# Kernel optimization log

Hardware: AMD Instinct MI355X
Metric: run time of the kernel (lower is better)

Reference implementation:

```python
import jax, jax.numpy as jnp
import numpy as np

CTX = 5  # context_len

def z_vector(x, ctx):
    # x: [B, L, E] -> [B, L, ctx*E]; slot j holds embedding of token (idx + j - ctx//2), zero-padded at edges
    half = ctx // 2
    B, L, E = x.shape
    xp = jnp.pad(x, ((0, 0), (half, half), (0, 0)))
    return jnp.concatenate([xp[:, i:i + L, :] for i in range(ctx)], axis=-1)

def setup_inputs() -> dict:
    key = jax.random.key(0)
    kq, ka, kw, kb = jax.random.split(key, 4)
    B, LQ, LA, E, F = 256, 64, 256, 300, 512
    question = jax.random.normal(kq, (B, LQ, E), dtype=jnp.float32)
    answer = jax.random.normal(ka, (B, LA, E), dtype=jnp.float32)
    W = jax.random.normal(kw, (CTX * E, F), dtype=jnp.float32) * 0.02
    b = jax.random.normal(kb, (F,), dtype=jnp.float32) * 0.02
    return {"question": question, "answer": answer, "W": W, "b": b}

def reference(question, answer, W, b):
    # Conv2d(1, F, (ctx*E, 1)) over the full-height Z vector == per-position linear map
    def branch(x):
        z = z_vector(x, CTX)                       # [B, L, ctx*E]
        out = jnp.einsum('blk,kf->bfl', z, W)      # [B, F, L]
        return out + b[None, :, None]
    return branch(question), branch(answer)
```

## Files before the change

kernel.cpp:

```cpp
#include <hip/hip_runtime.h>

#define NB   256
#define E0   300
#define EP   304
#define F_   512
#define KP   1536
#define NKT  48
#define LQ_  64
#define LA_  256

typedef __attribute__((ext_vector_type(4))) float f32x4;
typedef __attribute__((ext_vector_type(8))) short short8;

#define XQ_ELEMS (NB * (LQ_ + 4) * EP)
#define XA_ELEMS (NB * (LA_ + 4) * EP)
#define WF_ELEMS (F_ * KP)
#define OUTQ_ELEMS ((size_t)NB * F_ * LQ_)

__device__ __forceinline__ unsigned short f2bf(float x) {
    unsigned int u = __float_as_uint(x);
    u = u + 0x7fffu + ((u >> 16) & 1u);
    return (unsigned short)(u >> 16);
}

__global__ void prep_x(const float* __restrict__ q, const float* __restrict__ a,
                       unsigned short* __restrict__ xq, unsigned short* __restrict__ xa)
{
    const int row = blockIdx.x;
    const int tid = threadIdx.x;
    if (tid >= 76) return;
    const float* src;
    unsigned short* dst;
    bool valid;
    if (row < NB * (LQ_ + 4)) {
        int b = row / (LQ_ + 4), lp = row - b * (LQ_ + 4);
        dst = xq + (size_t)row * EP;
        valid = (lp >= 2 && lp < 2 + LQ_);
        src = q + ((size_t)b * LQ_ + (lp - 2)) * E0;
    } else {
        int r2 = row - NB * (LQ_ + 4);
        int b = r2 / (LA_ + 4), lp = r2 - b * (LA_ + 4);
        dst = xa + (size_t)r2 * EP;
        valid = (lp >= 2 && lp < 2 + LA_);
        src = a + ((size_t)b * LA_ + (lp - 2)) * E0;
    }
    unsigned long long pk = 0ull;
    if (valid && tid < 75) {
        const float4 v = reinterpret_cast<const float4*>(src)[tid];
        pk = (unsigned long long)f2bf(v.x)
           | ((unsigned long long)f2bf(v.y) << 16)
           | ((unsigned long long)f2bf(v.z) << 32)
           | ((unsigned long long)f2bf(v.w) << 48);
    }
    *reinterpret_cast<unsigned long long*>(dst + (size_t)tid * 4) = pk;
}

__global__ void prep_w2(const float* __restrict__ W, unsigned short* __restrict__ wfr)
{
    int idx = blockIdx.x * 256 + threadIdx.x;
    int j    = idx & 7;
    int lane = (idx >> 3) & 63;
    int chunk = idx >> 9;
    int kc = chunk % NKT;
    int tile16 = chunk / NKT;
    int f  = tile16 * 16 + (lane & 15);
    int kp = kc * 32 + (lane >> 4) * 8 + j;
    int jj = kp / EP;
    int e  = kp - jj * EP;
    float v = (kp < 5 * EP && e < E0) ? W[(size_t)(jj * E0 + e) * F_ + f] : 0.f;
    wfr[idx] = f2bf(v);
}

__global__ __launch_bounds__(256, 2) void qa_gemm(
    const unsigned short* __restrict__ xq,
    const unsigned short* __restrict__ xa,
    const unsigned short* __restrict__ wfr,
    const float* __restrict__ bias,
    float* __restrict__ out)
{
    __shared__ __align__(16) unsigned short lds[4 * 4096];

    const int bid = blockIdx.x;
    const int wg  = (bid & 7) * 160 + (bid >> 3);

    const unsigned short* xp;
    float* ob;
    int Mbase, lsh, Lp, ftBase;
    if (wg < 256) {
        Mbase  = (wg >> 1) * 128;
        ftBase = (wg & 1) * 256;
        xp = xq; lsh = 6; Lp = LQ_ + 4;
        ob = out;
    } else {
        const int id = wg - 256;
        Mbase  = (id >> 1) * 128;
        ftBase = (id & 1) * 256;
        xp = xa; lsh = 8; Lp = LA_ + 4;
        ob = out + OUTQ_ELEMS;
    }
    const int Lv = 1 << lsh;

    const int tid  = threadIdx.x;
    const int lane = tid & 63;
    const int wid  = tid >> 6;
    const int lq   = lane >> 4;
    const int lr   = lane & 15;

    const int s_c  = (lane & 3) ^ ((lane >> 3) & 3);
    const int sub  = lane >> 2;
    const int mr0 = Mbase + wid * 32 + sub, mr1 = mr0 + 16;
    const unsigned short* gZ0 = xp + (size_t)((mr0 >> lsh) * Lp + (mr0 & (Lv - 1))) * EP + s_c * 8;
    const unsigned short* gZ1 = xp + (size_t)((mr1 >> lsh) * Lp + (mr1 & (Lv - 1))) * EP + s_c * 8;
    const int dz0 = wid * 1024, dz1 = dz0 + 512;

#define GLLDS(p, d) __builtin_amdgcn_global_load_lds(                               \
        (const __attribute__((address_space(1))) void*)(p),                         \
        (__attribute__((address_space(3))) void*)(d), 16, 0, 0)
#define STAGE_Z(T) do { const int rb = ((T) & 3) * 4096; const size_t ko = (size_t)(T) * 32; \
    GLLDS(gZ0 + ko, lds + dz0 + rb); GLLDS(gZ1 + ko, lds + dz1 + rb); } while (0)

    const unsigned short* wpc0 = wfr + (size_t)((ftBase >> 4) + wid * 4 + 0) * NKT * 512 + lane * 8;
    const unsigned short* wpc1 = wfr + (size_t)((ftBase >> 4) + wid * 4 + 1) * NKT * 512 + lane * 8;
    const unsigned short* wpc2 = wfr + (size_t)((ftBase >> 4) + wid * 4 + 2) * NKT * 512 + lane * 8;
    const unsigned short* wpc3 = wfr + (size_t)((ftBase >> 4) + wid * 4 + 3) * NKT * 512 + lane * 8;

#define WLOAD(dst, p) do {                                                           \
    asm volatile("global_load_dwordx4 %0, %1, off" : "=v"(dst) : "v"(p) : "memory"); \
    (p) += 512; } while (0)

    const int cs = (lq ^ ((lr >> 1) & 3)) * 16;
    int zoff[8];
#pragma unroll
    for (int n = 0; n < 8; ++n) zoff[n] = (n * 16 + lr) * 64 + cs;

    f32x4 acc[4][8] = {};
    short8 WA0, WA1, WA2, WA3, WB0, WB1, WB2, WB3;

#define MFMA(a, b, c) __builtin_amdgcn_mfma_f32_16x16x32_bf16((a), (b), (c), 0, 0, 0)

#define KSTEP(T, C0, C1, C2, C3, N0, N1, N2, N3, DO_W, DO_Z, MIDW) do {             \
    const char* bb = (const char*)lds + ((T) & 3) * 8192;                           \
    short8 bA[4], bB[4];                                                            \
    _Pragma("unroll") for (int n = 0; n < 4; ++n) bA[n] = *(const short8*)(bb + zoff[n]); \
    if (DO_W) { WLOAD(N0, wpc0); WLOAD(N1, wpc1); WLOAD(N2, wpc2); WLOAD(N3, wpc3); } \
    if (DO_Z) { STAGE_Z((T) + 3); }                                                 \
    asm volatile("s_barrier\n\ts_waitcnt vmcnt(" #MIDW ") lgkmcnt(0)" ::: "memory"); \
    __builtin_amdgcn_sched_barrier(0);                                              \
    __builtin_amdgcn_s_setprio(1);                                                  \
    _Pragma("unroll") for (int n = 0; n < 4; ++n) {                                 \
        acc[0][n] = MFMA(C0, bA[n], acc[0][n]);                                     \
        acc[1][n] = MFMA(C1, bA[n], acc[1][n]);                                     \
        acc[2][n] = MFMA(C2, bA[n], acc[2][n]);                                     \
        acc[3][n] = MFMA(C3, bA[n], acc[3][n]);                                     \
    }                                                                               \
    __builtin_amdgcn_s_setprio(0);                                                  \
    __builtin_amdgcn_sched_barrier(0);                                              \
    _Pragma("unroll") for (int n = 0; n < 4; ++n) bB[n] = *(const short8*)(bb + zoff[4 + n]); \
    asm volatile("s_barrier\n\ts_waitcnt lgkmcnt(0)" ::: "memory");                 \
    __builtin_amdgcn_sched_barrier(0);                                              \
    __builtin_amdgcn_s_setprio(1);                                                  \
    _Pragma("unroll") for (int n = 0; n < 4; ++n) {                                 \
        acc[0][4 + n] = MFMA(C0, bB[n], acc[0][4 + n]);                             \
        acc[1][4 + n] = MFMA(C1, bB[n], acc[1][4 + n]);                             \
        acc[2][4 + n] = MFMA(C2, bB[n], acc[2][4 + n]);                             \
        acc[3][4 + n] = MFMA(C3, bB[n], acc[3][4 + n]);                             \
    }                                                                               \
    __builtin_amdgcn_s_setprio(0);                                                  \
    __builtin_amdgcn_sched_barrier(0);                                              \
} while (0)

#define ENDFENCE(N) asm volatile("s_waitcnt vmcnt(" #N ")\n\ts_barrier" ::: "memory")

    WLOAD(WA0, wpc0); WLOAD(WA1, wpc1); WLOAD(WA2, wpc2); WLOAD(WA3, wpc3);
    STAGE_Z(0); STAGE_Z(1); STAGE_Z(2);
    ENDFENCE(4);

    for (int i = 0; i < 22; ++i) {
        const int t = 2 * i;
        KSTEP(t,     WA0, WA1, WA2, WA3, WB0, WB1, WB2, WB3, 1, 1, 8);
        ENDFENCE(12);
        KSTEP(t + 1, WB0, WB1, WB2, WB3, WA0, WA1, WA2, WA3, 1, 1, 8);
        ENDFENCE(12);
    }
    KSTEP(44, WA0, WA1, WA2, WA3, WB0, WB1, WB2, WB3, 1, 1, 8);
    ENDFENCE(12);
    KSTEP(45, WB0, WB1, WB2, WB3, WA0, WA1, WA2, WA3, 1, 0, 6);
    ENDFENCE(10);
    KSTEP(46, WA0, WA1, WA2, WA3, WB0, WB1, WB2, WB3, 1, 0, 4);
    ENDFENCE(8);
    KSTEP(47, WB0, WB1, WB2, WB3, WA0, WA1, WA2, WA3, 0, 0, 0);

#undef KSTEP
#undef ENDFENCE
#undef WLOAD
#undef STAGE_Z
#undef GLLDS
#undef MFMA

#pragma unroll
    for (int ns = 0; ns < 8; ++ns) {
        const int m = Mbase + ns * 16 + lr;
        const int b = m >> lsh;
        const int l = m & (Lv - 1);
        float* orow = ob + ((size_t)b * F_ << lsh) + l;
#pragma unroll
        for (int ms = 0; ms < 4; ++ms) {
            const int f0 = ftBase + wid * 64 + ms * 16 + lq * 4;
            const f32x4 v = acc[ms][ns];
#pragma unroll
            for (int r = 0; r < 4; ++r)
                orow[(size_t)(f0 + r) << lsh] = v[r] + __ldg(&bias[f0 + r]);
        }
    }
}

extern "C" void kernel_launch(void* const* d_in, const int* in_sizes, int n_in,
                              void* d_out, int out_size, void* d_ws, size_t ws_size,
                              hipStream_t stream)
{
    const float* q    = (const float*)d_in[0];
    const float* a    = (const float*)d_in[1];
    const float* W    = (const float*)d_in[2];
    const float* bias = (const float*)d_in[3];
    float* out = (float*)d_out;

    unsigned short* xq  = (unsigned short*)d_ws;
    unsigned short* xa  = xq + XQ_ELEMS;
    unsigned short* wfr = xa + XA_ELEMS;

    const int xrows = NB * (LQ_ + 4) + NB * (LA_ + 4);
    prep_x<<<xrows, 128, 0, stream>>>(q, a, xq, xa);
    prep_w2<<<WF_ELEMS / 256, 256, 0, stream>>>(W, wfr);
    qa_gemm<<<1280, 256, 0, stream>>>(xq, xa, wfr, bias, out);
}
```

Before: 167.5 us.

## Halve GEMM M-tile to 64 rows, raise occupancy, flatten prep_x threads

New measurement: 175.9 us. +5.0%, slower.

```diff
diff --git a/kernel.cpp b/kernel.cpp
--- a/kernel.cpp
+++ b/kernel.cpp
@@ -16,6 +16,7 @@
 #define XA_ELEMS (NB * (LA_ + 4) * EP)
 #define WF_ELEMS (F_ * KP)
 #define OUTQ_ELEMS ((size_t)NB * F_ * LQ_)
+#define XROWS (NB * (LQ_ + 4) + NB * (LA_ + 4))
 
 __device__ __forceinline__ unsigned short f2bf(float x) {
     unsigned int u = __float_as_uint(x);
@@ -26,9 +27,11 @@
 __global__ void prep_x(const float* __restrict__ q, const float* __restrict__ a,
                        unsigned short* __restrict__ xq, unsigned short* __restrict__ xa)
 {
-    const int row = blockIdx.x;
-    const int tid = threadIdx.x;
-    if (tid >= 76) return;
+    int idx = blockIdx.x * 256 + threadIdx.x;
+    if (idx >= XROWS * 76) return;
+    int row = idx / 76;
+    int col = idx - row * 76;
+
     const float* src;
     unsigned short* dst;
     bool valid;
@@ -45,14 +48,14 @@
         src = a + ((size_t)b * LA_ + (lp - 2)) * E0;
     }
     unsigned long long pk = 0ull;
-    if (valid && tid < 75) {
-        const float4 v = reinterpret_cast<const float4*>(src)[tid];
+    if (valid && col < 75) {
+        const float4 v = reinterpret_cast<const float4*>(src)[col];
         pk = (unsigned long long)f2bf(v.x)
            | ((unsigned long long)f2bf(v.y) << 16)
            | ((unsigned long long)f2bf(v.z) << 32)
            | ((unsigned long long)f2bf(v.w) << 48);
     }
-    *reinterpret_cast<unsigned long long*>(dst + (size_t)tid * 4) = pk;
+    *reinterpret_cast<unsigned long long*>(dst + (size_t)col * 4) = pk;
 }
 
 __global__ void prep_w2(const float* __restrict__ W, unsigned short* __restrict__ wfr)
@@ -71,29 +74,29 @@
     wfr[idx] = f2bf(v);
 }
 
-__global__ __launch_bounds__(256, 2) void qa_gemm(
+__global__ __launch_bounds__(256, 3) void qa_gemm(
     const unsigned short* __restrict__ xq,
     const unsigned short* __restrict__ xa,
     const unsigned short* __restrict__ wfr,
     const float* __restrict__ bias,
     float* __restrict__ out)
 {
-    __shared__ __align__(16) unsigned short lds[4 * 4096];
+    __shared__ __align__(16) unsigned short lds[4 * 2048];
 
     const int bid = blockIdx.x;
-    const int wg  = (bid & 7) * 160 + (bid >> 3);
+    const int wg  = (bid & 7) * 320 + (bid >> 3);
 
     const unsigned short* xp;
     float* ob;
     int Mbase, lsh, Lp, ftBase;
-    if (wg < 256) {
-        Mbase  = (wg >> 1) * 128;
+    if (wg < 512) {
+        Mbase  = (wg >> 1) * 64;
         ftBase = (wg & 1) * 256;
         xp = xq; lsh = 6; Lp = LQ_ + 4;
         ob = out;
     } else {
-        const int id = wg - 256;
-        Mbase  = (id >> 1) * 128;
+        const int id = wg - 512;
+        Mbase  = (id >> 1) * 64;
         ftBase = (id & 1) * 256;
         xp = xa; lsh = 8; Lp = LA_ + 4;
         ob = out + OUTQ_ELEMS;
@@ -108,16 +111,15 @@
 
     const int s_c  = (lane & 3) ^ ((lane >> 3) & 3);
     const int sub  = lane >> 2;
-    const int mr0 = Mbase + wid * 32 + sub, mr1 = mr0 + 16;
+    const int mr0 = Mbase + wid * 16 + sub;
     const unsigned short* gZ0 = xp + (size_t)((mr0 >> lsh) * Lp + (mr0 & (Lv - 1))) * EP + s_c * 8;
-    const unsigned short* gZ1 = xp + (size_t)((mr1 >> lsh) * Lp + (mr1 & (Lv - 1))) * EP + s_c * 8;
-    const int dz0 = wid * 1024, dz1 = dz0 + 512;
+    const int dz0 = wid * 512;
 
 #define GLLDS(p, d) __builtin_amdgcn_global_load_lds(                               \
         (const __attribute__((address_space(1))) void*)(p),                         \
         (__attribute__((address_space(3))) void*)(d), 16, 0, 0)
-#define STAGE_Z(T) do { const int rb = ((T) & 3) * 4096; const size_t ko = (size_t)(T) * 32; \
-    GLLDS(gZ0 + ko, lds + dz0 + rb); GLLDS(gZ1 + ko, lds + dz1 + rb); } while (0)
+#define STAGE_Z(T) do { const int rb = ((T) & 3) * 2048; const size_t ko = (size_t)(T) * 32; \
+    GLLDS(gZ0 + ko, lds + dz0 + rb); } while (0)
 
     const unsigned short* wpc0 = wfr + (size_t)((ftBase >> 4) + wid * 4 + 0) * NKT * 512 + lane * 8;
     const unsigned short* wpc1 = wfr + (size_t)((ftBase >> 4) + wid * 4 + 1) * NKT * 512 + lane * 8;
@@ -129,76 +131,68 @@
     (p) += 512; } while (0)
 
     const int cs = (lq ^ ((lr >> 1) & 3)) * 16;
-    int zoff[8];
-#pragma unroll
-    for (int n = 0; n < 8; ++n) zoff[n] = (n * 16 + lr) * 64 + cs;
-
-    f32x4 acc[4][8] = {};
+    int zoff[4];
+#pragma unroll
+    for (int n = 0; n < 4; ++n) zoff[n] = (n * 16 + lr) * 64 + cs;
+
+    f32x4 acc[4][4] = {};
     short8 WA0, WA1, WA2, WA3, WB0, WB1, WB2, WB3;
 
 #define MFMA(a, b, c) __builtin_amdgcn_mfma_f32_16x16x32_bf16((a), (b), (c), 0, 0, 0)
 
-#define KSTEP(T, C0, C1, C2, C3, N0, N1, N2, N3, DO_W, DO_Z, MIDW) do {             \
-    const char* bb = (const char*)lds + ((T) & 3) * 8192;                           \
-    short8 bA[4], bB[4];                                                            \
-    _Pragma("unroll") for (int n = 0; n < 4; ++n) bA[n] = *(const short8*)(bb + zoff[n]); \
+#define KSTEP(T, C0, C1, C2, C3, N0, N1, N2, N3, DO_W, DO_Z, AV) do {               \
+    const char* bb = (const char*)lds + ((T) & 3) * 4096;                           \
+    short8 z01[2], z23[2];                                                          \
+    _Pragma("unroll") for (int n = 0; n < 2; ++n) z01[n] = *(const short8*)(bb + zoff[n]); \
     if (DO_W) { WLOAD(N0, wpc0); WLOAD(N1, wpc1); WLOAD(N2, wpc2); WLOAD(N3, wpc3); } \
     if (DO_Z) { STAGE_Z((T) + 3); }                                                 \
-    asm volatile("s_barrier\n\ts_waitcnt vmcnt(" #MIDW ") lgkmcnt(0)" ::: "memory"); \
+    asm volatile("s_waitcnt vmcnt(" #AV ") lgkmcnt(0)" ::: "memory");               \
     __builtin_amdgcn_sched_barrier(0);                                              \
     __builtin_amdgcn_s_setprio(1);                                                  \
-    _Pragma("unroll") for (int n = 0; n < 4; ++n) {                                 \
-        acc[0][n] = MFMA(C0, bA[n], acc[0][n]);                                     \
-        acc[1][n] = MFMA(C1, bA[n], acc[1][n]);                                     \
-        acc[2][n] = MFMA(C2, bA[n], acc[2][n]);                                     \
-        acc[3][n] = MFMA(C3, bA[n], acc[3][n]);                                     \
+    _Pragma("unroll") for (int n = 0; n < 2; ++n) {                                 \
+        acc[0][n] = MFMA(C0, z01[n], acc[0][n]);                                    \
+        acc[1][n] = MFMA(C1, z01[n], acc[1][n]);                                    \
+        acc[2][n] = MFMA(C2, z01[n], acc[2][n]);                                    \
+        acc[3][n] = MFMA(C3, z01[n], acc[3][n]);                                    \
     }                                                                               \
     __builtin_amdgcn_s_setprio(0);                                                  \
     __builtin_amdgcn_sched_barrier(0);                                              \
-    _Pragma("unroll") for (int n = 0; n < 4; ++n) bB[n] = *(const short8*)(bb + zoff[4 + n]); \
-    asm volatile("s_barrier\n\ts_waitcnt lgkmcnt(0)" ::: "memory");                 \
+    _Pragma("unroll") for (int n = 0; n < 2; ++n) z23[n] = *(const short8*)(bb + zoff[2 + n]); \
+    asm volatile("s_waitcnt lgkmcnt(0)\n\ts_barrier" ::: "memory");                 \
     __builtin_amdgcn_sched_barrier(0);                                              \
     __builtin_amdgcn_s_setprio(1);                                                  \
-    _Pragma("unroll") for (int n = 0; n < 4; ++n) {                                 \
-        acc[0][4 + n] = MFMA(C0, bB[n], acc[0][4 + n]);                             \
-        acc[1][4 + n] = MFMA(C1, bB[n], acc[1][4 + n]);                             \
-        acc[2][4 + n] = MFMA(C2, bB[n], acc[2][4 + n]);                             \
-        acc[3][4 + n] = MFMA(C3, bB[n], acc[3][4 + n]);                             \
+    _Pragma("unroll") for (int n = 0; n < 2; ++n) {                                 \
+        acc[0][2 + n] = MFMA(C0, z23[n], acc[0][2 + n]);                            \
+        acc[1][2 + n] = MFMA(C1, z23[n], acc[1][2 + n]);                            \
+        acc[2][2 + n] = MFMA(C2, z23[n], acc[2][2 + n]);                            \
+        acc[3][2 + n] = MFMA(C3, z23[n], acc[3][2 + n]);                            \
     }                                                                               \
     __builtin_amdgcn_s_setprio(0);                                                  \
     __builtin_amdgcn_sched_barrier(0);                                              \
 } while (0)
 
-#define ENDFENCE(N) asm volatile("s_waitcnt vmcnt(" #N ")\n\ts_barrier" ::: "memory")
-
     WLOAD(WA0, wpc0); WLOAD(WA1, wpc1); WLOAD(WA2, wpc2); WLOAD(WA3, wpc3);
     STAGE_Z(0); STAGE_Z(1); STAGE_Z(2);
-    ENDFENCE(4);
+    asm volatile("s_waitcnt vmcnt(2)\n\ts_barrier" ::: "memory");
 
     for (int i = 0; i < 22; ++i) {
         const int t = 2 * i;
-        KSTEP(t,     WA0, WA1, WA2, WA3, WB0, WB1, WB2, WB3, 1, 1, 8);
-        ENDFENCE(12);
-        KSTEP(t + 1, WB0, WB1, WB2, WB3, WA0, WA1, WA2, WA3, 1, 1, 8);
-        ENDFENCE(12);
-    }
-    KSTEP(44, WA0, WA1, WA2, WA3, WB0, WB1, WB2, WB3, 1, 1, 8);
-    ENDFENCE(12);
-    KSTEP(45, WB0, WB1, WB2, WB3, WA0, WA1, WA2, WA3, 1, 0, 6);
-    ENDFENCE(10);
+        KSTEP(t,     WA0, WA1, WA2, WA3, WB0, WB1, WB2, WB3, 1, 1, 6);
+        KSTEP(t + 1, WB0, WB1, WB2, WB3, WA0, WA1, WA2, WA3, 1, 1, 6);
+    }
+    KSTEP(44, WA0, WA1, WA2, WA3, WB0, WB1, WB2, WB3, 1, 1, 6);
+    KSTEP(45, WB0, WB1, WB2, WB3, WA0, WA1, WA2, WA3, 1, 0, 5);
     KSTEP(46, WA0, WA1, WA2, WA3, WB0, WB1, WB2, WB3, 1, 0, 4);
-    ENDFENCE(8);
     KSTEP(47, WB0, WB1, WB2, WB3, WA0, WA1, WA2, WA3, 0, 0, 0);
 
 #undef KSTEP
-#undef ENDFENCE
 #undef WLOAD
 #undef STAGE_Z
 #undef GLLDS
 #undef MFMA
 
 #pragma unroll
-    for (int ns = 0; ns < 8; ++ns) {
+    for (int ns = 0; ns < 4; ++ns) {
         const int m = Mbase + ns * 16 + lr;
         const int b = m >> lsh;
         const int l = m & (Lv - 1);
@@ -228,8 +222,7 @@
     unsigned short* xa  = xq + XQ_ELEMS;
     unsigned short* wfr = xa + XA_ELEMS;
 
-    const int xrows = NB * (LQ_ + 4) + NB * (LA_ + 4);
-    prep_x<<<xrows, 128, 0, stream>>>(q, a, xq, xa);
+    prep_x<<<(XROWS * 76 + 255) / 256, 256, 0, stream>>>(q, a, xq, xa);
     prep_w2<<<WF_ELEMS / 256, 256, 0, stream>>>(W, wfr);
-    qa_gemm<<<1280, 256, 0, stream>>>(xq, xa, wfr, bias, out);
-}
+    qa_gemm<<<2560, 256, 0, stream>>>(xq, xa, wfr, bias, out);
+}
```
